# Performance work log

Measured on AMD Instinct MI355X. Metric: run time of the kernel, lower is better.

## Reference

```python
import jax, jax.numpy as jnp
import numpy as np

TOP_K = 2


def setup_inputs() -> dict:
    key = jax.random.key(0)
    ks = jax.random.split(key, 6)
    B, S, D, F, E = 4, 2048, 1024, 4096, 8
    sd = 1.0 / np.sqrt(D)
    sf = 1.0 / np.sqrt(F)
    return {
        "x": jax.random.normal(ks[0], (B, S, D), dtype=jnp.float32),
        "gate_w": jax.random.normal(ks[1], (D, E), dtype=jnp.float32) * sd,
        "w1": jax.random.normal(ks[2], (E, D, F), dtype=jnp.float32) * sd,
        "b1": jax.random.normal(ks[3], (E, F), dtype=jnp.float32) * 0.01,
        "w2": jax.random.normal(ks[4], (E, F, D), dtype=jnp.float32) * sf,
        "b2": jax.random.normal(ks[5], (E, D), dtype=jnp.float32) * 0.01,
    }


def reference(x, gate_w, w1, b1, w2, b2):
    B, S, D = x.shape
    E = gate_w.shape[1]
    xf = x.reshape(-1, D)                        # [T, D], T = B*S
    T = xf.shape[0]

    # Gating: top-k logits, softmax over the selected k (in fp32, as in torch)
    logits = xf @ gate_w                         # [T, E]
    top_vals, top_idx = jax.lax.top_k(logits, TOP_K)            # [T, K]
    wts = jax.nn.softmax(top_vals.astype(jnp.float32), axis=-1).astype(x.dtype)

    # Dense combine weights: combine[t, e] = sum_k wts[t,k] * [top_idx[t,k]==e]
    rows = jnp.arange(T)[:, None]
    combine = jnp.zeros((T, E), dtype=x.dtype).at[rows, top_idx].add(wts)

    # Expert FFNs (dropout is identity in eval; torch GELU default = exact erf)
    out = jnp.zeros_like(xf)
    for e in range(E):
        h = jax.nn.gelu(xf @ w1[e] + b1[e], approximate=False)  # [T, F]
        out = out + combine[:, e:e + 1] * (h @ w2[e] + b2[e])
    return out.reshape(B, S, D)
```

## Files before the change

### kernel.cpp

```cpp
#include <hip/hip_runtime.h>


#define T_TOK 8192
#define D_DIM 1024
#define F_DIM 4096
#define E_NUM 8
#define BM 256
#define BN 256
#define BK 64
#define NK1 (D_DIM / BK)
#define NK2 (F_DIM / BK)
#define NX1 (F_DIM / BN)
#define NX2 (D_DIM / BN)
#define MAX_TILES (T_TOK * 2 / BM + E_NUM)
#define BM2 128
#define MAX_TILES2 (T_TOK * 2 / BM2 + E_NUM)

typedef float f32x4 __attribute__((ext_vector_type(4)));
typedef short bf16x8 __attribute__((ext_vector_type(8)));
typedef unsigned short u16x8 __attribute__((ext_vector_type(8)));

__device__ __forceinline__ unsigned short f2bf(float f) {
  union { float f; unsigned u; } v; v.f = f;
  unsigned r = v.u + 0x7FFFu + ((v.u >> 16) & 1u);
  return (unsigned short)(r >> 16);
}

__device__ __forceinline__ void async_cp16(const unsigned short* g, unsigned short* l) {
  __builtin_amdgcn_global_load_lds((__attribute__((address_space(1))) void*)g,
                                   (__attribute__((address_space(3))) void*)l,
                                   16, 0, 0);
}

#define WAIT_VM6 asm volatile("s_waitcnt vmcnt(6)" ::: "memory")
#define WAIT_VM4 asm volatile("s_waitcnt vmcnt(4)" ::: "memory")
#define WAIT_LGKM0 asm volatile("s_waitcnt lgkmcnt(0)" ::: "memory")
#define RAW_BARRIER asm volatile("s_barrier" ::: "memory")


__global__ __launch_bounds__(256) void transpose_cast_kernel(
    const float* __restrict__ src, unsigned short* __restrict__ dst,
    int R, int C) {
  __shared__ float tile[64][65];
  int e = blockIdx.z;
  src += (size_t)e * R * C;
  dst += (size_t)e * R * C;
  int c0 = blockIdx.x * 64;
  int r0 = blockIdx.y * 64;
  int t = threadIdx.x;
  int cl = (t & 15) * 4, rl = t >> 4;
#pragma unroll
  for (int i = 0; i < 4; ++i) {
    int r = rl + i * 16;
    float4 v = *(const float4*)(src + (size_t)(r0 + r) * C + c0 + cl);
    tile[r][cl + 0] = v.x;
    tile[r][cl + 1] = v.y;
    tile[r][cl + 2] = v.z;
    tile[r][cl + 3] = v.w;
  }
  __syncthreads();
  int rl2 = (t & 7) * 8, cl2 = t >> 3;
#pragma unroll
  for (int i = 0; i < 2; ++i) {
    int c = cl2 + i * 32;
    u16x8 o;
#pragma unroll
    for (int k = 0; k < 8; ++k) o[k] = f2bf(tile[rl2 + k][c]);
    *(u16x8*)(dst + (size_t)(c0 + c) * R + r0 + rl2) = o;
  }
}

__global__ __launch_bounds__(256) void gate_kernel(
    const float* __restrict__ x, const float* __restrict__ gw,
    float* __restrict__ topk_w, int* __restrict__ topk_e,
    unsigned short* __restrict__ xb) {
  int t = (blockIdx.x * 256 + threadIdx.x) >> 6;
  int lane = threadIdx.x & 63;
  const float* xr = x + (size_t)t * D_DIM;
  unsigned short* xbr = xb + (size_t)t * D_DIM;
  float acc[8];
#pragma unroll
  for (int e = 0; e < 8; ++e) acc[e] = 0.f;
  for (int j = 0; j < D_DIM / 64; ++j) {
    int d = lane + 64 * j;
    float xv = xr[d];
    xbr[d] = f2bf(xv);
    float4 g0 = ((const float4*)(gw + (size_t)d * 8))[0];
    float4 g1 = ((const float4*)(gw + (size_t)d * 8))[1];
    acc[0] += xv * g0.x; acc[1] += xv * g0.y;
    acc[2] += xv * g0.z; acc[3] += xv * g0.w;
    acc[4] += xv * g1.x; acc[5] += xv * g1.y;
    acc[6] += xv * g1.z; acc[7] += xv * g1.w;
  }
#pragma unroll
  for (int off = 32; off > 0; off >>= 1) {
#pragma unroll
    for (int e = 0; e < 8; ++e) acc[e] += __shfl_xor(acc[e], off);
  }
  if (lane == 0) {
    int e0 = 0; float v0 = acc[0];
#pragma unroll
    for (int e = 1; e < 8; ++e)
      if (acc[e] > v0) { v0 = acc[e]; e0 = e; }
    int e1 = -1; float v1 = -1e30f;
#pragma unroll
    for (int e = 0; e < 8; ++e)
      if (e != e0 && acc[e] > v1) { v1 = acc[e]; e1 = e; }
    float ex = expf(v1 - v0);
    float inv = 1.f / (1.f + ex);
    topk_w[2 * t] = inv;
    topk_w[2 * t + 1] = ex * inv;
    topk_e[2 * t] = e0;
    topk_e[2 * t + 1] = e1;
  }
}

__global__ void scatter_kernel(const int* __restrict__ topk_e,
                               int* __restrict__ cnt, int* __restrict__ assign) {
  int idx = blockIdx.x * blockDim.x + threadIdx.x;
  int e = topk_e[idx];
  int lane = threadIdx.x & 63;
#pragma unroll
  for (int ex = 0; ex < E_NUM; ++ex) {
    unsigned long long m = __ballot(e == ex);
    if (e == ex) {
      int src = __ffsll((unsigned long long)m) - 1;
      int nbefore = __popcll(m & ((1ull << lane) - 1ull));
      int base = 0;
      if (lane == src) base = atomicAdd(&cnt[ex], __popcll(m));
      base = __shfl(base, src);
      assign[ex * T_TOK + base + nbefore] = idx;
    }
  }
}

__global__ void tiles_kernel(const int* __restrict__ cnt,
                             int* __restrict__ ndesc, int4* __restrict__ desc,
                             int4* __restrict__ desc2) {
  if (threadIdx.x != 0) return;
  int nt = 0, nt2 = 0, hb = 0;
  for (int e = 0; e < E_NUM; ++e) {
    int c = cnt[e];
    for (int s = 0; s < c; s += BM) {
      int4 d;
      d.x = e; d.y = s; d.z = hb;
      d.w = (c - s < BM) ? (c - s) : BM;
      desc[nt++] = d;
    }
    for (int s = 0; s < c; s += BM2) {
      int4 d;
      d.x = e; d.y = s; d.z = hb;
      d.w = (c - s < BM2) ? (c - s) : BM2;
      desc2[nt2++] = d;
    }
    hb += c;
  }
  ndesc[0] = nt;
  ndesc[1] = nt2;
}


__global__ __launch_bounds__(512, 2) void gemm1_kernel(
    const unsigned short* __restrict__ xb, const unsigned short* __restrict__ w1t,
    const float* __restrict__ b1, const int* __restrict__ assign,
    const int* __restrict__ ndesc, const int4* __restrict__ desc,
    unsigned short* __restrict__ H) {
  const int nwg = NX1 * MAX_TILES;
  int lin = blockIdx.y * NX1 + blockIdx.x;
  int wg = (lin & 7) * (nwg >> 3) + (lin >> 3);
  int tileid = wg / NX1;
  int n0 = (wg & (NX1 - 1)) * BN;
  if (tileid >= ndesc[0]) return;
  int4 dc = desc[tileid];
  int e = dc.x, start = dc.y, hbase = dc.z, mcnt = dc.w;

  extern __shared__ __attribute__((aligned(16))) unsigned short smem[];

  int tid = threadIdx.x, lane = tid & 63, wv = tid >> 6;

  int drow = tid >> 3, dcc = tid & 7;
  int g = (dcc - drow) & 7;
  const unsigned short* gAr[4];
  const unsigned short* gBr[4];
#pragma unroll
  for (int j = 0; j < 4; ++j) {
    int r = drow + 64 * j;
    int rc = r < mcnt ? r : (mcnt - 1);
    int a = assign[e * T_TOK + start + rc];
    gAr[j] = xb + (size_t)(a >> 1) * D_DIM + g * 8;
    gBr[j] = w1t + (size_t)(e * F_DIM + n0 + r) * D_DIM + g * 8;
  }
  int ldst = wv * 512;

  int kc16 = lane >> 4, r16 = lane & 15;
  int m_off = (wv & 1) * 128, n_off = (wv >> 1) * 64;

  f32x4 acc[8][4];
#pragma unroll
  for (int i = 0; i < 8; ++i)
#pragma unroll
    for (int j = 0; j < 4; ++j) acc[i][j] = (f32x4){0.f, 0.f, 0.f, 0.f};
  bf16x8 bfr[4][2];

  auto issueA = [&](int t, int j) {
    int kt = t < NK1 ? t : NK1 - 1;
    async_cp16(gAr[j] + kt * 64, smem + (t & 1) * 32768 + ldst + j * 4096);
  };
  auto issueB = [&](int t, int j) {
    int kt = t < NK1 ? t : NK1 - 1;
    async_cp16(gBr[j] + kt * 64, smem + (t & 1) * 32768 + 16384 + ldst + j * 4096);
  };

  auto phase = [&](int t, int q) {
    const unsigned short* Ab = smem + (t & 1) * 32768;
    const unsigned short* Bb = Ab + 16384;
    if (q == 0) {
#pragma unroll
      for (int j = 0; j < 4; ++j) {
        int rb = n_off + j * 16 + r16;
#pragma unroll
        for (int h = 0; h < 2; ++h)
          bfr[j][h] = *(const bf16x8*)(Bb + rb * 64 + ((h * 4 + kc16 + rb) & 7) * 8);
      }
    }
    bf16x8 af[2][2];
#pragma unroll
    for (int m2 = 0; m2 < 2; ++m2) {
      int ra = m_off + (2 * q + m2) * 16 + r16;
#pragma unroll
      for (int h = 0; h < 2; ++h)
        af[m2][h] = *(const bf16x8*)(Ab + ra * 64 + ((h * 4 + kc16 + ra) & 7) * 8);
    }
    if (q == 0)      { issueA(t + 1, 1); issueA(t + 1, 3); }
    else if (q == 1) { issueB(t + 2, 0); issueB(t + 2, 1); }
    else if (q == 2) { issueB(t + 2, 2); issueB(t + 2, 3); }
    else             { issueA(t + 2, 0); issueA(t + 2, 2); }
    WAIT_LGKM0;
    __builtin_amdgcn_s_setprio(1);
#pragma unroll
    for (int h = 0; h < 2; ++h)
#pragma unroll
      for (int m2 = 0; m2 < 2; ++m2)
#pragma unroll
        for (int j = 0; j < 4; ++j)
          acc[2 * q + m2][j] = __builtin_amdgcn_mfma_f32_16x16x32_bf16(
              af[m2][h], bfr[j][h], acc[2 * q + m2][j], 0, 0, 0);
    __builtin_amdgcn_s_setprio(0);
    if (q == 3) WAIT_VM6;
    RAW_BARRIER;
  };

#pragma unroll
  for (int j = 0; j < 4; ++j) issueB(0, j);
#pragma unroll
  for (int j = 0; j < 4; ++j) issueA(0, j);
  issueB(1, 0); issueB(1, 1); issueB(1, 2); issueB(1, 3);
  issueA(1, 0); issueA(1, 2);
  WAIT_VM6;
  RAW_BARRIER;

  for (int t = 0; t < NK1; ++t) {
    phase(t, 0); phase(t, 1); phase(t, 2); phase(t, 3);
  }

  int col = lane & 15, rbase = (lane >> 4) * 4;
  float bias[4];
#pragma unroll
  for (int j = 0; j < 4; ++j) bias[j] = b1[e * F_DIM + n0 + n_off + j * 16 + col];
#pragma unroll
  for (int i = 0; i < 8; ++i) {
#pragma unroll
    for (int rg = 0; rg < 4; ++rg) {
      int r = m_off + i * 16 + rbase + rg;
      if (r < mcnt) {
        unsigned short* hrow = H + (size_t)(hbase + start + r) * F_DIM + n0 + n_off + col;
#pragma unroll
        for (int j = 0; j < 4; ++j) {
          float v = acc[i][j][rg] + bias[j];
          v = 0.5f * v * (1.0f + erff(v * 0.70710678118654752f));
          hrow[j * 16] = f2bf(v);
        }
      }
    }
  }
}


__global__ __launch_bounds__(512, 2) void gemm2_kernel(
    const unsigned short* __restrict__ H, const unsigned short* __restrict__ w2t,
    const float* __restrict__ b2, const int* __restrict__ assign,
    const float* __restrict__ topk_w,
    const int* __restrict__ ndesc, const int4* __restrict__ desc2,
    float* __restrict__ out) {
  const int nwg = NX2 * MAX_TILES2;
  int lin = blockIdx.y * NX2 + blockIdx.x;
  int wg = (lin & 7) * (nwg >> 3) + (lin >> 3);
  int tileid = wg / NX2;
  int n0 = (wg & (NX2 - 1)) * BN;
  if (tileid >= ndesc[1]) return;
  int4 dc = desc2[tileid];
  int e = dc.x, start = dc.y, hbase = dc.z, mcnt = dc.w;

  extern __shared__ __attribute__((aligned(16))) unsigned short smem[];

  int tid = threadIdx.x, lane = tid & 63, wv = tid >> 6;

  int drow = tid >> 3, dcc = tid & 7;
  int g = (dcc - drow) & 7;
  const unsigned short* gA2[2];
  const unsigned short* gB2[4];
#pragma unroll
  for (int j = 0; j < 2; ++j) {
    int r = (drow & 31) + (drow >> 5) * 64 + j * 32;
    int rc = r < mcnt ? r : (mcnt - 1);
    gA2[j] = H + (size_t)(hbase + start + rc) * F_DIM + g * 8;
  }
#pragma unroll
  for (int j = 0; j < 4; ++j) {
    int r = drow + j * 64;
    gB2[j] = w2t + (size_t)(e * D_DIM + n0 + r) * F_DIM + g * 8;
  }
  int arowbase = ((wv * 8) & 31) + ((wv * 8) >> 5) * 64;
  int ldstB = wv * 512;

  int kc16 = lane >> 4, r16 = lane & 15;
  int m_off = (wv & 1) * 64, n_off = (wv >> 1) * 64;

  f32x4 acc[4][4];
#pragma unroll
  for (int i = 0; i < 4; ++i)
#pragma unroll
    for (int j = 0; j < 4; ++j) acc[i][j] = (f32x4){0.f, 0.f, 0.f, 0.f};
  bf16x8 bfr[4][2];

  auto issueA = [&](int t, int j) {
    int kt = t < NK2 ? t : NK2 - 1;
    async_cp16(gA2[j] + kt * 64,
               smem + (t & 1) * 24576 + (arowbase + j * 32) * 64);
  };
  auto issueB = [&](int t, int j) {
    int kt = t < NK2 ? t : NK2 - 1;
    async_cp16(gB2[j] + kt * 64,
               smem + (t & 1) * 24576 + 8192 + ldstB + j * 4096);
  };

  auto phase = [&](int t, int q) {
    const unsigned short* Ab = smem + (t & 1) * 24576;
    const unsigned short* Bb = Ab + 8192;
    if (q == 0) {
#pragma unroll
      for (int j = 0; j < 4; ++j) {
        int rb = n_off + j * 16 + r16;
#pragma unroll
        for (int h = 0; h < 2; ++h)
          bfr[j][h] = *(const bf16x8*)(Bb + rb * 64 + ((h * 4 + kc16 + rb) & 7) * 8);
      }
    }
    bf16x8 af[2][2];
#pragma unroll
    for (int m2 = 0; m2 < 2; ++m2) {
      int ra = m_off + (2 * q + m2) * 16 + r16;
#pragma unroll
      for (int h = 0; h < 2; ++h)
        af[m2][h] = *(const bf16x8*)(Ab + ra * 64 + ((h * 4 + kc16 + ra) & 7) * 8);
    }
    if (q == 0) { issueB(t + 1, 3); issueA(t + 1, 1); }
    else        { issueB(t + 2, 0); issueB(t + 2, 1); issueB(t + 2, 2); issueA(t + 2, 0); }
    WAIT_LGKM0;
    __builtin_amdgcn_s_setprio(1);
#pragma unroll
    for (int h = 0; h < 2; ++h)
#pragma unroll
      for (int m2 = 0; m2 < 2; ++m2)
#pragma unroll
        for (int j = 0; j < 4; ++j)
          acc[2 * q + m2][j] = __builtin_amdgcn_mfma_f32_16x16x32_bf16(
              af[m2][h], bfr[j][h], acc[2 * q + m2][j], 0, 0, 0);
    __builtin_amdgcn_s_setprio(0);
    if (q == 1) WAIT_VM4;
    RAW_BARRIER;
  };

  issueB(0, 0); issueB(0, 1); issueB(0, 2); issueB(0, 3);
  issueA(0, 0); issueA(0, 1);
  issueB(1, 0); issueB(1, 1); issueB(1, 2);
  issueA(1, 0);
  WAIT_VM4;
  RAW_BARRIER;

  for (int t = 0; t < NK2; ++t) { phase(t, 0); phase(t, 1); }

  int col = lane & 15, rbase = (lane >> 4) * 4;
  float bias[4];
#pragma unroll
  for (int j = 0; j < 4; ++j) bias[j] = b2[e * D_DIM + n0 + n_off + j * 16 + col];
#pragma unroll
  for (int i = 0; i < 4; ++i) {
#pragma unroll
    for (int rg = 0; rg < 4; ++rg) {
      int r = m_off + i * 16 + rbase + rg;
      if (r < mcnt) {
        int a = assign[e * T_TOK + start + r];
        float wt = topk_w[a];
        float* orow = out + (size_t)(a >> 1) * D_DIM + n0 + n_off + col;
#pragma unroll
        for (int j = 0; j < 4; ++j) {
          float v = acc[i][j][rg] + bias[j];
          atomicAdd(orow + j * 16, wt * v);
        }
      }
    }
  }
}


extern "C" void kernel_launch(void* const* d_in, const int* in_sizes, int n_in,
                              void* d_out, int out_size, void* d_ws, size_t ws_size,
                              hipStream_t stream) {
  const float* x      = (const float*)d_in[0];
  const float* gate_w = (const float*)d_in[1];
  const float* w1     = (const float*)d_in[2];
  const float* b1     = (const float*)d_in[3];
  const float* w2     = (const float*)d_in[4];
  const float* b2     = (const float*)d_in[5];
  float* out = (float*)d_out;

  char* ws = (char*)d_ws;
  size_t off = 0;
  auto alloc = [&](size_t bytes) {
    char* p = ws + off;
    off = (off + bytes + 255) & ~(size_t)255;
    return p;
  };
  unsigned short* xb   = (unsigned short*)alloc((size_t)T_TOK * D_DIM * 2);
  unsigned short* w1t  = (unsigned short*)alloc((size_t)E_NUM * D_DIM * F_DIM * 2);
  unsigned short* w2t  = (unsigned short*)alloc((size_t)E_NUM * D_DIM * F_DIM * 2);
  unsigned short* Hbuf = (unsigned short*)alloc((size_t)2 * T_TOK * F_DIM * 2);
  float* topk_w = (float*)alloc((size_t)2 * T_TOK * 4);
  int* topk_e   = (int*)alloc((size_t)2 * T_TOK * 4);
  int* assign   = (int*)alloc((size_t)E_NUM * T_TOK * 4);
  int* cnt      = (int*)alloc(64);
  int* ndesc    = (int*)alloc(64);
  int4* desc    = (int4*)alloc((size_t)MAX_TILES * 16);
  int4* desc2   = (int4*)alloc((size_t)MAX_TILES2 * 16);

  hipFuncSetAttribute(reinterpret_cast<const void*>(gemm1_kernel),
                      hipFuncAttributeMaxDynamicSharedMemorySize, 131072);
  hipFuncSetAttribute(reinterpret_cast<const void*>(gemm2_kernel),
                      hipFuncAttributeMaxDynamicSharedMemorySize, 98304);

  hipMemsetAsync(cnt, 0, 64, stream);
  hipMemsetAsync(out, 0, (size_t)out_size * 4, stream);

  transpose_cast_kernel<<<dim3(F_DIM / 64, D_DIM / 64, E_NUM), 256, 0, stream>>>(
      w1, w1t, D_DIM, F_DIM);
  transpose_cast_kernel<<<dim3(D_DIM / 64, F_DIM / 64, E_NUM), 256, 0, stream>>>(
      w2, w2t, F_DIM, D_DIM);
  gate_kernel<<<T_TOK / 4, 256, 0, stream>>>(x, gate_w, topk_w, topk_e, xb);
  scatter_kernel<<<2 * T_TOK / 256, 256, 0, stream>>>(topk_e, cnt, assign);
  tiles_kernel<<<1, 64, 0, stream>>>(cnt, ndesc, desc, desc2);
  gemm1_kernel<<<dim3(NX1, MAX_TILES), 512, 131072, stream>>>(
      xb, w1t, b1, assign, ndesc, desc, Hbuf);
  gemm2_kernel<<<dim3(NX2, MAX_TILES2), 512, 98304, stream>>>(
      Hbuf, w2t, b2, assign, topk_w, ndesc, desc2, out);
}
```

Baseline: 860.9 us.

## Restructure GEMM1 into two half-phases, defer LDS waits, and use polynomial erf GELU

GEMM1's inner loop goes from four quarter-phases per K-tile to two half-phases. Each half loads more A fragments at once and issues its async copies in bigger batches, which halves the barriers per K-tile. Both GEMM kernels now wait on lgkmcnt after the MFMA block instead of before it, so LDS reads can overlap issue, and they drain vmcnt before the epilogue. The exact erff in the GELU is replaced by the Abramowitz-Stegun polynomial plus __expf, which is cheaper but only accurate to about 1e-7 absolute error; it also relies on the compiler inserting waits for the LDS fragments it uses.

```diff
diff --git a/kernel.cpp b/kernel.cpp
--- a/kernel.cpp
+++ b/kernel.cpp
@@ -26,6 +26,17 @@
   return (unsigned short)(r >> 16);
 }
 
+__device__ __forceinline__ float gelu_f(float v) {
+  float z = v * 0.70710678118654752f;
+  float az = fabsf(z);
+  float t = 1.0f / (1.0f + 0.3275911f * az);
+  float p = ((((1.061405429f * t - 1.453152027f) * t + 1.421413741f) * t
+              - 0.284496736f) * t + 0.254829592f) * t;
+  float E = 1.0f - p * __expf(-az * az);
+  float er = z < 0.f ? -E : E;
+  return 0.5f * v * (1.0f + er);
+}
+
 __device__ __forceinline__ void async_cp16(const unsigned short* g, unsigned short* l) {
   __builtin_amdgcn_global_load_lds((__attribute__((address_space(1))) void*)g,
                                    (__attribute__((address_space(3))) void*)l,
@@ -34,6 +45,7 @@
 
 #define WAIT_VM6 asm volatile("s_waitcnt vmcnt(6)" ::: "memory")
 #define WAIT_VM4 asm volatile("s_waitcnt vmcnt(4)" ::: "memory")
+#define WAIT_VM0 asm volatile("s_waitcnt vmcnt(0)" ::: "memory")
 #define WAIT_LGKM0 asm volatile("s_waitcnt lgkmcnt(0)" ::: "memory")
 #define RAW_BARRIER asm volatile("s_barrier" ::: "memory")
 
@@ -211,42 +223,62 @@
     async_cp16(gBr[j] + kt * 64, smem + (t & 1) * 32768 + 16384 + ldst + j * 4096);
   };
 
-  auto phase = [&](int t, int q) {
+  auto half0 = [&](int t) {
     const unsigned short* Ab = smem + (t & 1) * 32768;
     const unsigned short* Bb = Ab + 16384;
-    if (q == 0) {
-#pragma unroll
-      for (int j = 0; j < 4; ++j) {
-        int rb = n_off + j * 16 + r16;
-#pragma unroll
-        for (int h = 0; h < 2; ++h)
-          bfr[j][h] = *(const bf16x8*)(Bb + rb * 64 + ((h * 4 + kc16 + rb) & 7) * 8);
-      }
-    }
-    bf16x8 af[2][2];
-#pragma unroll
-    for (int m2 = 0; m2 < 2; ++m2) {
-      int ra = m_off + (2 * q + m2) * 16 + r16;
+#pragma unroll
+    for (int j = 0; j < 4; ++j) {
+      int rb = n_off + j * 16 + r16;
 #pragma unroll
       for (int h = 0; h < 2; ++h)
-        af[m2][h] = *(const bf16x8*)(Ab + ra * 64 + ((h * 4 + kc16 + ra) & 7) * 8);
-    }
-    if (q == 0)      { issueA(t + 1, 1); issueA(t + 1, 3); }
-    else if (q == 1) { issueB(t + 2, 0); issueB(t + 2, 1); }
-    else if (q == 2) { issueB(t + 2, 2); issueB(t + 2, 3); }
-    else             { issueA(t + 2, 0); issueA(t + 2, 2); }
+        bfr[j][h] = *(const bf16x8*)(Bb + rb * 64 + ((h * 4 + kc16 + rb) & 7) * 8);
+    }
+    bf16x8 af[4][2];
+#pragma unroll
+    for (int m = 0; m < 4; ++m) {
+      int ra = m_off + m * 16 + r16;
+#pragma unroll
+      for (int h = 0; h < 2; ++h)
+        af[m][h] = *(const bf16x8*)(Ab + ra * 64 + ((h * 4 + kc16 + ra) & 7) * 8);
+    }
+    issueA(t + 1, 1); issueA(t + 1, 3);
+    __builtin_amdgcn_s_setprio(1);
+#pragma unroll
+    for (int h = 0; h < 2; ++h)
+#pragma unroll
+      for (int m = 0; m < 4; ++m)
+#pragma unroll
+        for (int j = 0; j < 4; ++j)
+          acc[m][j] = __builtin_amdgcn_mfma_f32_16x16x32_bf16(
+              af[m][h], bfr[j][h], acc[m][j], 0, 0, 0);
+    __builtin_amdgcn_s_setprio(0);
     WAIT_LGKM0;
+    RAW_BARRIER;
+  };
+  auto half1 = [&](int t) {
+    const unsigned short* Ab = smem + (t & 1) * 32768;
+    bf16x8 af[4][2];
+#pragma unroll
+    for (int m = 0; m < 4; ++m) {
+      int ra = m_off + (4 + m) * 16 + r16;
+#pragma unroll
+      for (int h = 0; h < 2; ++h)
+        af[m][h] = *(const bf16x8*)(Ab + ra * 64 + ((h * 4 + kc16 + ra) & 7) * 8);
+    }
+    issueB(t + 2, 0); issueB(t + 2, 1); issueB(t + 2, 2); issueB(t + 2, 3);
+    issueA(t + 2, 0); issueA(t + 2, 2);
     __builtin_amdgcn_s_setprio(1);
 #pragma unroll
     for (int h = 0; h < 2; ++h)
 #pragma unroll
-      for (int m2 = 0; m2 < 2; ++m2)
+      for (int m = 0; m < 4; ++m)
 #pragma unroll
         for (int j = 0; j < 4; ++j)
-          acc[2 * q + m2][j] = __builtin_amdgcn_mfma_f32_16x16x32_bf16(
-              af[m2][h], bfr[j][h], acc[2 * q + m2][j], 0, 0, 0);
+          acc[4 + m][j] = __builtin_amdgcn_mfma_f32_16x16x32_bf16(
+              af[m][h], bfr[j][h], acc[4 + m][j], 0, 0, 0);
     __builtin_amdgcn_s_setprio(0);
-    if (q == 3) WAIT_VM6;
+    WAIT_VM6;
+    WAIT_LGKM0;
     RAW_BARRIER;
   };
 
@@ -259,9 +291,8 @@
   WAIT_VM6;
   RAW_BARRIER;
 
-  for (int t = 0; t < NK1; ++t) {
-    phase(t, 0); phase(t, 1); phase(t, 2); phase(t, 3);
-  }
+  for (int t = 0; t < NK1; ++t) { half0(t); half1(t); }
+  WAIT_VM0;
 
   int col = lane & 15, rbase = (lane >> 4) * 4;
   float bias[4];
@@ -276,8 +307,7 @@
         unsigned short* hrow = H + (size_t)(hbase + start + r) * F_DIM + n0 + n_off + col;
 #pragma unroll
         for (int j = 0; j < 4; ++j) {
-          float v = acc[i][j][rg] + bias[j];
-          v = 0.5f * v * (1.0f + erff(v * 0.70710678118654752f));
+          float v = gelu_f(acc[i][j][rg] + bias[j]);
           hrow[j * 16] = f2bf(v);
         }
       }
@@ -366,7 +396,6 @@
     }
     if (q == 0) { issueB(t + 1, 3); issueA(t + 1, 1); }
     else        { issueB(t + 2, 0); issueB(t + 2, 1); issueB(t + 2, 2); issueA(t + 2, 0); }
-    WAIT_LGKM0;
     __builtin_amdgcn_s_setprio(1);
 #pragma unroll
     for (int h = 0; h < 2; ++h)
@@ -378,6 +407,7 @@
               af[m2][h], bfr[j][h], acc[2 * q + m2][j], 0, 0, 0);
     __builtin_amdgcn_s_setprio(0);
     if (q == 1) WAIT_VM4;
+    WAIT_LGKM0;
     RAW_BARRIER;
   };
 
@@ -389,6 +419,7 @@
   RAW_BARRIER;
 
   for (int t = 0; t < NK2; ++t) { phase(t, 0); phase(t, 1); }
+  WAIT_VM0;
 
   int col = lane & 15, rbase = (lane >> 4) * 4;
   float bias[4];
```

After: 845.9 us. No clear change (-1.7%).
